# Performance work log

Measured on AMD Instinct MI355X. Metric: run time of the kernel, lower is better.

The kernel has to match this reference:

```python
import jax, jax.numpy as jnp
import numpy as np

C = 256
K = 9
PAD = (K - 1) // 2  # 4


def setup_inputs() -> dict:
    key = jax.random.key(0)
    k1, k2, k3 = jax.random.split(key, 3)
    fea = jax.random.normal(k1, (8, C, 128, 128), dtype=jnp.float32)
    # Conv2d(C, C, (1,9)) with kernel height 1 -> 1D conv weight [O, I, K]
    fan_in = C * K
    bound = 1.0 / np.sqrt(fan_in)
    weight = jax.random.uniform(k2, (C, C, K), dtype=jnp.float32, minval=-bound, maxval=bound)
    bias = jax.random.uniform(k3, (C,), dtype=jnp.float32, minval=-bound, maxval=bound)
    return {"fea": fea, "weight": weight, "bias": bias}


def _conv_relu(x, weight, bias):
    # x: [n, c, w] -> 1D conv along width, then ReLU (matches Conv2d (1,9) on a 1-row slice)
    y = jax.lax.conv_general_dilated(
        x, weight, window_strides=(1,), padding=[(PAD, PAD)],
        dimension_numbers=("NCW", "OIW", "NCW"))
    return jax.nn.relu(y + bias[None, :, None])


def reference(fea, weight, bias):
    n, c, h, w = fea.shape
    rows = jnp.moveaxis(fea, 2, 0)  # [h, n, c, w]

    def step(carry, row):
        new = _conv_relu(carry, weight, bias) + row
        return new, new

    # forward (top-down) scan: fea_stack[i] = conv(fea_stack[i-1]) + fea_stack[i]
    _, ys_f = jax.lax.scan(step, rows[0], rows[1:])
    full = jnp.concatenate([rows[:1], ys_f], axis=0)  # [h, n, c, w]

    # backward (bottom-up) scan over i = h-2 .. 1
    mid = full[1:h - 1]
    _, ys_b = jax.lax.scan(step, full[h - 1], mid[::-1])
    out_rows = jnp.concatenate([full[:1], ys_b[::-1], full[h - 1:]], axis=0)

    return jnp.moveaxis(out_rows, 0, 2)  # back to [n, c, h, w]
```

## Files before the change

kernel.cpp:

```cpp
#include <hip/hip_runtime.h>

typedef _Float16 f16;
typedef _Float16 f16x8 __attribute__((ext_vector_type(8)));
typedef _Float16 f16x4 __attribute__((ext_vector_type(4)));
typedef float    f32x4 __attribute__((ext_vector_type(4)));
typedef float    f32x16 __attribute__((ext_vector_type(16)));
typedef unsigned long long u64;

#define N_   8
#define C_   256
#define H_   128
#define W_   128
#define K_   9
#define PAD_ 4
#define WP_  136

#define WELEMS (8*9*16*64*8)
#define XT_SZ  (N_*WP_*256)
#define XBUF_F16 (N_*WP_*512)
#define NBLK   256
#define NSTEP  253
#define LDS_BYTES (40960 + 32768 + 128)

__device__ __host__ inline int xpos(int ci, int wp) {
    int g = ((ci >> 3) + 5 * wp) & 31;
    return g * 8 + (ci & 7);
}

__global__ __launch_bounds__(256) void prep_w(const float* __restrict__ w,
                                              f16* __restrict__ wh, f16* __restrict__ wl) {
    int t = blockIdx.x * 256 + threadIdx.x;
    if (t >= WELEMS) return;
    int j = t & 7;      int q = t >> 3;
    int lane = q & 63;  q >>= 6;
    int c = q & 15;     q >>= 4;
    int k = q % 9;      int ct = q / 9;
    int co = ct * 32 + (lane & 31);
    int ci = c * 16 + (lane >> 5) * 8 + j;
    float wf = w[(co * C_ + ci) * K_ + k];
    f16 hi = (f16)wf;
    f16 lo = (f16)(wf - (float)hi);
    wh[t] = hi;  wl[t] = lo;
}

__global__ __launch_bounds__(256) void prep_x0(const float* __restrict__ fea,
                                               f16* __restrict__ xb0, f16* __restrict__ xb1) {
    int t = blockIdx.x * 256 + threadIdx.x;
    if (t >= XT_SZ) return;
    int ci = t & 255;
    int wp = (t >> 8) % WP_;
    int n  = t / (WP_ * 256);
    int w  = wp - PAD_;
    bool pad = (unsigned)w >= (unsigned)W_;
    float v = pad ? 0.0f : fea[((size_t)(n * C_ + ci) * H_ + 0) * W_ + w];
    f16 hi = (f16)v;
    f16 lo = (f16)(v - (float)hi);
    size_t row = ((size_t)n * WP_ + wp) * 512;
    int p = xpos(ci, wp);
    xb0[row + p] = hi;  xb0[row + 256 + p] = lo;
    if (pad) { xb1[row + p] = (f16)0.f; xb1[row + 256 + p] = (f16)0.f; }
}

__global__ __launch_bounds__(256) void copy_row0(const float* __restrict__ fea,
                                                 float* __restrict__ out) {
    int idx = blockIdx.x * 256 + threadIdx.x;
    if (idx >= N_ * C_ * W_) return;
    int w = idx % W_;
    int nc = idx / W_;
    size_t off = (size_t)nc * (H_ * W_) + w;
    out[off] = fea[off];
}

#define TIE(x) asm volatile("" : "+v"(x))

__global__ __launch_bounds__(512, 2)
void conv_persist(
    f16* __restrict__ xb0, f16* __restrict__ xb1,
    const f16* __restrict__ whp, const f16* __restrict__ wlp,
    const float* __restrict__ bias, const float* __restrict__ fea,
    float* out, unsigned* ctr)
{
    extern __shared__ unsigned char Xs[];
    f32x4*    red  = (f32x4*)(Xs + 40960);
    unsigned* wcnt = (unsigned*)(Xs + 40960 + 32768);

    const int b   = blockIdx.x;
    const int n   = b & 7;
    const int ct  = (b >> 3) & 7;
    const int wq  = b >> 6;
    const int w0  = wq * 32;
    const int tid = threadIdx.x;
    const int wv  = tid >> 6;
    const int l   = tid & 63;
    const int m   = l & 31;
    const int hh  = l >> 5;
    unsigned* flags = ctr + n * 64;
    const int bslot = b >> 3;

    if (tid == 0) *wcnt = 0;

    f16x8 wkh[9][2], wkl[9][2];
    #pragma unroll
    for (int k = 0; k < 9; ++k)
        #pragma unroll
        for (int cs = 0; cs < 2; ++cs) {
            size_t o = ((((size_t)ct * 9 + k) * 16 + (wv * 2 + cs)) * 64 + l) * 8;
            wkh[k][cs] = *(const f16x8*)&whp[o];
            wkl[k][cs] = *(const f16x8*)&wlp[o];
        }
    #pragma unroll
    for (int k = 0; k < 9; ++k)
        #pragma unroll
        for (int cs = 0; cs < 2; ++cs) { TIE(wkh[k][cs]); TIE(wkl[k][cs]); }
    __syncthreads();

    const int dq = wv & 3;
    const int co_base = ct * 32 + dq * 8 + hh * 4;
    const size_t HW = (size_t)H_ * W_;
    float4 bv = *(const float4*)&bias[co_base];
    const float bvr[4] = {bv.x, bv.y, bv.z, bv.w};

    for (int step = 0; step < NSTEP; ++step) {
        const int  cur   = step & 1;
        const bool fwd   = step < 127;
        const int  h_out = fwd ? (step + 1) : (NSTEP - step);
        const float* radd = fwd ? fea : out;
        const size_t obase = (((size_t)(n * C_ + co_base)) * H_ + h_out) * W_ + w0 + m;
        f16* xcur = cur ? xb1 : xb0;
        f16* xnxt = cur ? xb0 : xb1;

        {
            const u64* src = (const u64*)(xcur + ((size_t)n * WP_ + w0) * 512);
            u64 va[5], vb2[5];
            #pragma unroll
            for (int ii = 0; ii < 5; ++ii) {
                int g = tid + ii * 512;
                va[ii]  = __hip_atomic_load(src + (size_t)g * 2,     __ATOMIC_RELAXED, __HIP_MEMORY_SCOPE_AGENT);
                vb2[ii] = __hip_atomic_load(src + (size_t)g * 2 + 1, __ATOMIC_RELAXED, __HIP_MEMORY_SCOPE_AGENT);
            }
            #pragma unroll
            for (int ii = 0; ii < 5; ++ii) {
                int g = tid + ii * 512;
                u64 p[2] = {va[ii], vb2[ii]};
                uint4 qd;
                __builtin_memcpy(&qd, p, 16);
                *(uint4*)(Xs + (size_t)g * 16) = qd;
            }
        }
        float rv[4] = {0.f, 0.f, 0.f, 0.f};
        if (wv < 4) {
            #pragma unroll
            for (int c2 = 0; c2 < 4; ++c2)
                rv[c2] = radd[obase + (size_t)c2 * HW];
        }
        __syncthreads();

        f32x16 a0v{}, crv{};
        #pragma unroll
        for (int k = 0; k < 9; ++k) {
            #pragma unroll
            for (int cs = 0; cs < 2; ++cs) {
                const int rl  = m + k;
                const int gsw = (((wv * 2 + cs) * 2 + hh + 5 * rl) & 31) * 16;
                const unsigned char* base = Xs + rl * 1024 + gsw;
                f16x8 bh = *(const f16x8*)base;
                f16x8 bl = *(const f16x8*)(base + 512);
                a0v = __builtin_amdgcn_mfma_f32_32x32x16_f16(wkh[k][cs], bh, a0v, 0, 0, 0);
                crv = __builtin_amdgcn_mfma_f32_32x32x16_f16(wkh[k][cs], bl, crv, 0, 0, 0);
                crv = __builtin_amdgcn_mfma_f32_32x32x16_f16(wkl[k][cs], bh, crv, 0, 0, 0);
            }
        }

        {
            f32x16 sp = a0v + crv;
            #pragma unroll
            for (int rq = 0; rq < 4; ++rq) {
                f32x4 qv = {sp[rq * 4 + 0], sp[rq * 4 + 1], sp[rq * 4 + 2], sp[rq * 4 + 3]};
                red[(wv * 4 + rq) * 64 + l] = qv;
            }
        }
        __syncthreads();

        if (wv < 4) {
            f32x4 s4 = red[(0 * 4 + dq) * 64 + l];
            #pragma unroll
            for (int cc = 1; cc < 8; ++cc)
                s4 += red[(cc * 4 + dq) * 64 + l];
            float y[4];
            #pragma unroll
            for (int c2 = 0; c2 < 4; ++c2)
                y[c2] = fmaxf(s4[c2] + bvr[c2], 0.0f) + rv[c2];

            if (step < NSTEP - 1) {
                const int wp = w0 + m + PAD_;
                const size_t row = ((size_t)n * WP_ + wp) * 512;
                const int g   = (ct * 4 + dq + 5 * wp) & 31;
                const int pos = g * 8 + hh * 4;
                f16x4 hv, lv;
                #pragma unroll
                for (int c2 = 0; c2 < 4; ++c2) {
                    f16 hi = (f16)y[c2];
                    hv[c2] = hi;
                    lv[c2] = (f16)(y[c2] - (float)hi);
                }
                u64 uh, ul;
                __builtin_memcpy(&uh, &hv, 8);
                __builtin_memcpy(&ul, &lv, 8);
                __hip_atomic_store((u64*)&xnxt[row + pos],       uh, __ATOMIC_RELAXED, __HIP_MEMORY_SCOPE_AGENT);
                __hip_atomic_store((u64*)&xnxt[row + 256 + pos], ul, __ATOMIC_RELAXED, __HIP_MEMORY_SCOPE_AGENT);
                asm volatile("s_waitcnt vmcnt(0)" ::: "memory");
                if (l == 0)
                    __hip_atomic_fetch_add(wcnt, 1u, __ATOMIC_RELAXED, __HIP_MEMORY_SCOPE_WORKGROUP);
                const unsigned tgt = (unsigned)(step + 1);
                if (wv == 0 && l == 0) {
                    while (__hip_atomic_load(wcnt, __ATOMIC_RELAXED, __HIP_MEMORY_SCOPE_WORKGROUP) < 4u * tgt) {}
                    __hip_atomic_store(flags + bslot, tgt, __ATOMIC_RELAXED, __HIP_MEMORY_SCOPE_AGENT);
                }
                #pragma unroll
                for (int c2 = 0; c2 < 4; ++c2)
                    out[obase + (size_t)c2 * HW] = y[c2];
                if (wv == 0) {
                    while (true) {
                        unsigned v = tgt;
                        if (l < 32)
                            v = __hip_atomic_load(flags + l, __ATOMIC_RELAXED, __HIP_MEMORY_SCOPE_AGENT);
                        if (__all((int)(v >= tgt))) break;
                    }
                }
            } else {
                #pragma unroll
                for (int c2 = 0; c2 < 4; ++c2)
                    out[obase + (size_t)c2 * HW] = y[c2];
            }
        }
        __syncthreads();
    }
}

__global__ __launch_bounds__(256) void step_f32(
    const float* __restrict__ xprev, const float* __restrict__ radd,
    float* __restrict__ yout, const float* __restrict__ wsrc,
    const float* __restrict__ bias, int h_prev, int h_out)
{
    __shared__ float XsF[C_][40];
    const int t  = threadIdx.x;
    const int bx = blockIdx.x;
    const int n  = bx & 7;
    const int wb = (bx >> 3) & 3;
    const int cb = bx >> 5;
    const int w0 = wb * 32;
    {
        const size_t nbase = (size_t)n * C_ * (H_ * W_) + (size_t)h_prev * W_;
        for (int idx = t; idx < C_ * 40; idx += 256) {
            int ci = idx / 40;
            int j  = idx - ci * 40;
            int w  = w0 - PAD_ + j;
            float v = 0.0f;
            if ((unsigned)w < (unsigned)W_)
                v = xprev[nbase + (size_t)ci * (H_ * W_) + w];
            XsF[ci][j] = v;
        }
    }
    __syncthreads();
    const int co = cb * 32 + (t >> 3);
    const int w4 = (t & 7) * 4;
    const float* wr = wsrc + (size_t)co * (C_ * K_);
    float acc0 = 0.f, acc1 = 0.f, acc2 = 0.f, acc3 = 0.f;
    for (int ci = 0; ci < C_; ci++) {
        float wk[K_];
        #pragma unroll
        for (int k = 0; k < K_; k++) wk[k] = wr[ci * K_ + k];
        float xv[12];
        float4 a = *(const float4*)&XsF[ci][w4];
        float4 bq = *(const float4*)&XsF[ci][w4 + 4];
        float4 c = *(const float4*)&XsF[ci][w4 + 8];
        xv[0]=a.x; xv[1]=a.y; xv[2]=a.z; xv[3]=a.w;
        xv[4]=bq.x; xv[5]=bq.y; xv[6]=bq.z; xv[7]=bq.w;
        xv[8]=c.x; xv[9]=c.y; xv[10]=c.z; xv[11]=c.w;
        #pragma unroll
        for (int k = 0; k < K_; k++) {
            acc0 = fmaf(wk[k], xv[k],     acc0);
            acc1 = fmaf(wk[k], xv[k + 1], acc1);
            acc2 = fmaf(wk[k], xv[k + 2], acc2);
            acc3 = fmaf(wk[k], xv[k + 3], acc3);
        }
    }
    const float bb = bias[co];
    const size_t obase = (((size_t)n * C_ + co) * H_ + h_out) * W_ + w0 + w4;
    float4 r = *(const float4*)&radd[obase];
    float4 o;
    o.x = fmaxf(acc0 + bb, 0.f) + r.x;
    o.y = fmaxf(acc1 + bb, 0.f) + r.y;
    o.z = fmaxf(acc2 + bb, 0.f) + r.z;
    o.w = fmaxf(acc3 + bb, 0.f) + r.w;
    *(float4*)&yout[obase] = o;
}

extern "C" void kernel_launch(void* const* d_in, const int* in_sizes, int n_in,
                              void* d_out, int out_size, void* d_ws, size_t ws_size,
                              hipStream_t stream) {
    const float* fea    = (const float*)d_in[0];
    const float* weight = (const float*)d_in[1];
    const float* bias   = (const float*)d_in[2];
    float* out = (float*)d_out;

    const size_t need = (size_t)2 * WELEMS * 2 + (size_t)2 * XBUF_F16 * 2 + 2048;

    copy_row0<<<(N_ * C_ * W_ + 255) / 256, 256, 0, stream>>>(fea, out);

    if (ws_size >= need && d_ws != nullptr) {
        f16* wh  = (f16*)d_ws;
        f16* wl  = wh + WELEMS;
        f16* xb0 = wl + WELEMS;
        f16* xb1 = xb0 + XBUF_F16;
        unsigned* ctr = (unsigned*)(xb1 + XBUF_F16);

        hipMemsetAsync(ctr, 0, 2048, stream);
        prep_w<<<(WELEMS + 255) / 256, 256, 0, stream>>>(weight, wh, wl);
        prep_x0<<<(XT_SZ + 255) / 256, 256, 0, stream>>>(fea, xb0, xb1);

        hipFuncSetAttribute((const void*)conv_persist,
                            hipFuncAttributeMaxDynamicSharedMemorySize, LDS_BYTES);
        conv_persist<<<NBLK, 512, LDS_BYTES, stream>>>(xb0, xb1, wh, wl, bias, fea, out, ctr);
    } else {
        for (int h = 1; h < H_; h++)
            step_f32<<<256, 256, 0, stream>>>(out, fea, out, weight, bias, h - 1, h);
        for (int h = H_ - 2; h >= 1; h--)
            step_f32<<<256, 256, 0, stream>>>(out, out, out, weight, bias, h + 1, h);
    }
}
```

Baseline: 1.341 ms.

## Split hi/lo activation staging into two LDS phases to overlap compute

Per step, the hi half of the activation window is written to LDS first and the hi-dependent MFMAs (wh*xh, wl*xh) run, then the lo half is stored to a separate LDS region and the wh*xl MFMAs run. This lets the lo stores sit behind the first MFMA batch and splits the single compensation accumulator into two independent chains. It adds a barrier per step, keeps more registers live across the first MFMA phase, and enlarges the LDS footprint, which could hurt occupancy with two blocks per CU.

After: 1.494 ms. +11.4%, slower.

```diff
diff --git a/kernel.cpp b/kernel.cpp
--- a/kernel.cpp
+++ b/kernel.cpp
@@ -20,7 +20,10 @@
 #define XBUF_F16 (N_*WP_*512)
 #define NBLK   256
 #define NSTEP  253
-#define LDS_BYTES (40960 + 32768 + 128)
+#define XS_LO  20480
+#define RED_OFF 40960
+#define WCNT_OFF 73728
+#define LDS_BYTES 84992
 
 __device__ __host__ inline int xpos(int ci, int wp) {
     int g = ((ci >> 3) + 5 * wp) & 31;
@@ -81,8 +84,8 @@
     float* out, unsigned* ctr)
 {
     extern __shared__ unsigned char Xs[];
-    f32x4*    red  = (f32x4*)(Xs + 40960);
-    unsigned* wcnt = (unsigned*)(Xs + 40960 + 32768);
+    f32x4*    red  = (f32x4*)(Xs + RED_OFF);
+    unsigned* wcnt = (unsigned*)(Xs + WCNT_OFF);
 
     const int b   = blockIdx.x;
     const int n   = b & 7;
@@ -129,23 +132,14 @@
         f16* xcur = cur ? xb1 : xb0;
         f16* xnxt = cur ? xb0 : xb1;
 
-        {
-            const u64* src = (const u64*)(xcur + ((size_t)n * WP_ + w0) * 512);
-            u64 va[5], vb2[5];
-            #pragma unroll
-            for (int ii = 0; ii < 5; ++ii) {
-                int g = tid + ii * 512;
-                va[ii]  = __hip_atomic_load(src + (size_t)g * 2,     __ATOMIC_RELAXED, __HIP_MEMORY_SCOPE_AGENT);
-                vb2[ii] = __hip_atomic_load(src + (size_t)g * 2 + 1, __ATOMIC_RELAXED, __HIP_MEMORY_SCOPE_AGENT);
-            }
-            #pragma unroll
-            for (int ii = 0; ii < 5; ++ii) {
-                int g = tid + ii * 512;
-                u64 p[2] = {va[ii], vb2[ii]};
-                uint4 qd;
-                __builtin_memcpy(&qd, p, 16);
-                *(uint4*)(Xs + (size_t)g * 16) = qd;
-            }
+        const u64* src = (const u64*)(xcur + ((size_t)n * WP_ + w0) * 512);
+        u64 vhi[5], vlo[5];
+        #pragma unroll
+        for (int ii = 0; ii < 5; ++ii) {
+            int idx = tid + ii * 512;
+            int row = idx >> 6, g = idx & 63;
+            vhi[ii] = __hip_atomic_load(src + (size_t)row * 128 + g,      __ATOMIC_RELAXED, __HIP_MEMORY_SCOPE_AGENT);
+            vlo[ii] = __hip_atomic_load(src + (size_t)row * 128 + 64 + g, __ATOMIC_RELAXED, __HIP_MEMORY_SCOPE_AGENT);
         }
         float rv[4] = {0.f, 0.f, 0.f, 0.f};
         if (wv < 4) {
@@ -153,26 +147,47 @@
             for (int c2 = 0; c2 < 4; ++c2)
                 rv[c2] = radd[obase + (size_t)c2 * HW];
         }
+        #pragma unroll
+        for (int ii = 0; ii < 5; ++ii) {
+            int idx = tid + ii * 512;
+            int row = idx >> 6, g = idx & 63;
+            *(u64*)(Xs + row * 512 + g * 8) = vhi[ii];
+        }
         __syncthreads();
 
-        f32x16 a0v{}, crv{};
+        f32x16 a0v{}, c1v{}, c2v{};
         #pragma unroll
         for (int k = 0; k < 9; ++k) {
             #pragma unroll
             for (int cs = 0; cs < 2; ++cs) {
                 const int rl  = m + k;
                 const int gsw = (((wv * 2 + cs) * 2 + hh + 5 * rl) & 31) * 16;
-                const unsigned char* base = Xs + rl * 1024 + gsw;
-                f16x8 bh = *(const f16x8*)base;
-                f16x8 bl = *(const f16x8*)(base + 512);
+                f16x8 bh = *(const f16x8*)(Xs + rl * 512 + gsw);
                 a0v = __builtin_amdgcn_mfma_f32_32x32x16_f16(wkh[k][cs], bh, a0v, 0, 0, 0);
-                crv = __builtin_amdgcn_mfma_f32_32x32x16_f16(wkh[k][cs], bl, crv, 0, 0, 0);
-                crv = __builtin_amdgcn_mfma_f32_32x32x16_f16(wkl[k][cs], bh, crv, 0, 0, 0);
+                c2v = __builtin_amdgcn_mfma_f32_32x32x16_f16(wkl[k][cs], bh, c2v, 0, 0, 0);
             }
         }
+        #pragma unroll
+        for (int ii = 0; ii < 5; ++ii) {
+            int idx = tid + ii * 512;
+            int row = idx >> 6, g = idx & 63;
+            *(u64*)(Xs + XS_LO + row * 512 + g * 8) = vlo[ii];
+        }
+        __syncthreads();
+
+        #pragma unroll
+        for (int k = 0; k < 9; ++k) {
+            #pragma unroll
+            for (int cs = 0; cs < 2; ++cs) {
+                const int rl  = m + k;
+                const int gsw = (((wv * 2 + cs) * 2 + hh + 5 * rl) & 31) * 16;
+                f16x8 bl = *(const f16x8*)(Xs + XS_LO + rl * 512 + gsw);
+                c1v = __builtin_amdgcn_mfma_f32_32x32x16_f16(wkh[k][cs], bl, c1v, 0, 0, 0);
+            }
+        }
 
         {
-            f32x16 sp = a0v + crv;
+            f32x16 sp = (a0v + c1v) + c2v;
             #pragma unroll
             for (int rq = 0; rq < 4; ++rq) {
                 f32x4 qv = {sp[rq * 4 + 0], sp[rq * 4 + 1], sp[rq * 4 + 2], sp[rq * 4 + 3]};
```

## Double block to 1024 threads, split channel reduction and roles across waves

Applied to the files above, without the earlier changes.

Each block now runs 16 waves, and each wave handles a single 16-input-channel chunk with one accumulator. This shortens the per-wave MFMA chain and the per-step critical path. Partial sums are reduced in two stages through LDS. Output stores, next-buffer stores with flag signalling, and the cross-block flag polling are assigned to separate wave groups so they overlap. It adds an extra barrier per step and more register pressure per CU.

Result: slower. 1.700 ms (+26.8%).

```diff
diff --git a/kernel.cpp b/kernel.cpp
--- a/kernel.cpp
+++ b/kernel.cpp
@@ -20,7 +20,9 @@
 #define XBUF_F16 (N_*WP_*512)
 #define NBLK   256
 #define NSTEP  253
-#define LDS_BYTES (40960 + 32768 + 128)
+#define RED_OFF  40960
+#define WCNT_OFF 73728
+#define LDS_BYTES 84992
 
 __device__ __host__ inline int xpos(int ci, int wp) {
     int g = ((ci >> 3) + 5 * wp) & 31;
@@ -73,7 +75,7 @@
 
 #define TIE(x) asm volatile("" : "+v"(x))
 
-__global__ __launch_bounds__(512, 2)
+__global__ __launch_bounds__(1024, 4)
 void conv_persist(
     f16* __restrict__ xb0, f16* __restrict__ xb1,
     const f16* __restrict__ whp, const f16* __restrict__ wlp,
@@ -81,8 +83,8 @@
     float* out, unsigned* ctr)
 {
     extern __shared__ unsigned char Xs[];
-    f32x4*    red  = (f32x4*)(Xs + 40960);
-    unsigned* wcnt = (unsigned*)(Xs + 40960 + 32768);
+    f32x4*    red  = (f32x4*)(Xs + RED_OFF);
+    unsigned* wcnt = (unsigned*)(Xs + WCNT_OFF);
 
     const int b   = blockIdx.x;
     const int n   = b & 7;
@@ -99,19 +101,15 @@
 
     if (tid == 0) *wcnt = 0;
 
-    f16x8 wkh[9][2], wkl[9][2];
+    f16x8 wkh[9], wkl[9];
     #pragma unroll
-    for (int k = 0; k < 9; ++k)
-        #pragma unroll
-        for (int cs = 0; cs < 2; ++cs) {
-            size_t o = ((((size_t)ct * 9 + k) * 16 + (wv * 2 + cs)) * 64 + l) * 8;
-            wkh[k][cs] = *(const f16x8*)&whp[o];
-            wkl[k][cs] = *(const f16x8*)&wlp[o];
-        }
+    for (int k = 0; k < 9; ++k) {
+        size_t o = ((((size_t)ct * 9 + k) * 16 + wv) * 64 + l) * 8;
+        wkh[k] = *(const f16x8*)&whp[o];
+        wkl[k] = *(const f16x8*)&wlp[o];
+    }
     #pragma unroll
-    for (int k = 0; k < 9; ++k)
-        #pragma unroll
-        for (int cs = 0; cs < 2; ++cs) { TIE(wkh[k][cs]); TIE(wkl[k][cs]); }
+    for (int k = 0; k < 9; ++k) { TIE(wkh[k]); TIE(wkl[k]); }
     __syncthreads();
 
     const int dq = wv & 3;
@@ -131,57 +129,56 @@
 
         {
             const u64* src = (const u64*)(xcur + ((size_t)n * WP_ + w0) * 512);
-            u64 va[5], vb2[5];
-            #pragma unroll
-            for (int ii = 0; ii < 5; ++ii) {
-                int g = tid + ii * 512;
-                va[ii]  = __hip_atomic_load(src + (size_t)g * 2,     __ATOMIC_RELAXED, __HIP_MEMORY_SCOPE_AGENT);
-                vb2[ii] = __hip_atomic_load(src + (size_t)g * 2 + 1, __ATOMIC_RELAXED, __HIP_MEMORY_SCOPE_AGENT);
-            }
-            #pragma unroll
-            for (int ii = 0; ii < 5; ++ii) {
-                int g = tid + ii * 512;
-                u64 p[2] = {va[ii], vb2[ii]};
-                uint4 qd;
-                __builtin_memcpy(&qd, p, 16);
-                *(uint4*)(Xs + (size_t)g * 16) = qd;
-            }
+            u64 v[5];
+            #pragma unroll
+            for (int ii = 0; ii < 5; ++ii)
+                v[ii] = __hip_atomic_load(src + (size_t)(tid + ii * 1024),
+                                          __ATOMIC_RELAXED, __HIP_MEMORY_SCOPE_AGENT);
+            #pragma unroll
+            for (int ii = 0; ii < 5; ++ii)
+                *(u64*)(Xs + (size_t)(tid + ii * 1024) * 8) = v[ii];
         }
         float rv[4] = {0.f, 0.f, 0.f, 0.f};
-        if (wv < 4) {
+        if (wv < 8) {
             #pragma unroll
             for (int c2 = 0; c2 < 4; ++c2)
                 rv[c2] = radd[obase + (size_t)c2 * HW];
         }
         __syncthreads();
 
-        f32x16 a0v{}, crv{};
+        f32x16 a{};
         #pragma unroll
         for (int k = 0; k < 9; ++k) {
-            #pragma unroll
-            for (int cs = 0; cs < 2; ++cs) {
-                const int rl  = m + k;
-                const int gsw = (((wv * 2 + cs) * 2 + hh + 5 * rl) & 31) * 16;
-                const unsigned char* base = Xs + rl * 1024 + gsw;
-                f16x8 bh = *(const f16x8*)base;
-                f16x8 bl = *(const f16x8*)(base + 512);
-                a0v = __builtin_amdgcn_mfma_f32_32x32x16_f16(wkh[k][cs], bh, a0v, 0, 0, 0);
-                crv = __builtin_amdgcn_mfma_f32_32x32x16_f16(wkh[k][cs], bl, crv, 0, 0, 0);
-                crv = __builtin_amdgcn_mfma_f32_32x32x16_f16(wkl[k][cs], bh, crv, 0, 0, 0);
+            const int rl  = m + k;
+            const int gsw = ((wv * 2 + hh + 5 * rl) & 31) * 16;
+            const unsigned char* base = Xs + rl * 1024 + gsw;
+            f16x8 bh = *(const f16x8*)base;
+            f16x8 bl = *(const f16x8*)(base + 512);
+            a = __builtin_amdgcn_mfma_f32_32x32x16_f16(wkh[k], bh, a, 0, 0, 0);
+            a = __builtin_amdgcn_mfma_f32_32x32x16_f16(wkh[k], bl, a, 0, 0, 0);
+            a = __builtin_amdgcn_mfma_f32_32x32x16_f16(wkl[k], bh, a, 0, 0, 0);
+        }
+
+        if (wv >= 8) {
+            #pragma unroll
+            for (int rq = 0; rq < 4; ++rq) {
+                f32x4 qv = {a[rq * 4 + 0], a[rq * 4 + 1], a[rq * 4 + 2], a[rq * 4 + 3]};
+                red[((wv - 8) * 4 + rq) * 64 + l] = qv;
             }
         }
-
-        {
-            f32x16 sp = a0v + crv;
+        __syncthreads();
+
+        if (wv < 8) {
             #pragma unroll
             for (int rq = 0; rq < 4; ++rq) {
-                f32x4 qv = {sp[rq * 4 + 0], sp[rq * 4 + 1], sp[rq * 4 + 2], sp[rq * 4 + 3]};
-                red[(wv * 4 + rq) * 64 + l] = qv;
+                f32x4 qv = {a[rq * 4 + 0], a[rq * 4 + 1], a[rq * 4 + 2], a[rq * 4 + 3]};
+                red[(wv * 4 + rq) * 64 + l] = qv + red[(wv * 4 + rq) * 64 + l];
             }
         }
         __syncthreads();
 
-        if (wv < 4) {
+        const unsigned tgt = (unsigned)(step + 1);
+        if (wv < 8) {
             f32x4 s4 = red[(0 * 4 + dq) * 64 + l];
             #pragma unroll
             for (int cc = 1; cc < 8; ++cc)
@@ -191,7 +188,11 @@
             for (int c2 = 0; c2 < 4; ++c2)
                 y[c2] = fmaxf(s4[c2] + bvr[c2], 0.0f) + rv[c2];
 
-            if (step < NSTEP - 1) {
+            if (wv < 4) {
+                #pragma unroll
+                for (int c2 = 0; c2 < 4; ++c2)
+                    out[obase + (size_t)c2 * HW] = y[c2];
+            } else if (step < NSTEP - 1) {
                 const int wp = w0 + m + PAD_;
                 const size_t row = ((size_t)n * WP_ + wp) * 512;
                 const int g   = (ct * 4 + dq + 5 * wp) & 31;
@@ -211,26 +212,17 @@
                 asm volatile("s_waitcnt vmcnt(0)" ::: "memory");
                 if (l == 0)
                     __hip_atomic_fetch_add(wcnt, 1u, __ATOMIC_RELAXED, __HIP_MEMORY_SCOPE_WORKGROUP);
-                const unsigned tgt = (unsigned)(step + 1);
-                if (wv == 0 && l == 0) {
+                if (wv == 4 && l == 0) {
                     while (__hip_atomic_load(wcnt, __ATOMIC_RELAXED, __HIP_MEMORY_SCOPE_WORKGROUP) < 4u * tgt) {}
                     __hip_atomic_store(flags + bslot, tgt, __ATOMIC_RELAXED, __HIP_MEMORY_SCOPE_AGENT);
                 }
-                #pragma unroll
-                for (int c2 = 0; c2 < 4; ++c2)
-                    out[obase + (size_t)c2 * HW] = y[c2];
-                if (wv == 0) {
-                    while (true) {
-                        unsigned v = tgt;
-                        if (l < 32)
-                            v = __hip_atomic_load(flags + l, __ATOMIC_RELAXED, __HIP_MEMORY_SCOPE_AGENT);
-                        if (__all((int)(v >= tgt))) break;
-                    }
-                }
-            } else {
-                #pragma unroll
-                for (int c2 = 0; c2 < 4; ++c2)
-                    out[obase + (size_t)c2 * HW] = y[c2];
+            }
+        } else if (wv == 8 && step < NSTEP - 1) {
+            while (true) {
+                unsigned v = tgt;
+                if (l < 32)
+                    v = __hip_atomic_load(flags + l, __ATOMIC_RELAXED, __HIP_MEMORY_SCOPE_AGENT);
+                if (__all((int)(v >= tgt))) break;
             }
         }
         __syncthreads();
@@ -321,7 +313,7 @@
 
         hipFuncSetAttribute((const void*)conv_persist,
                             hipFuncAttributeMaxDynamicSharedMemorySize, LDS_BYTES);
-        conv_persist<<<NBLK, 512, LDS_BYTES, stream>>>(xb0, xb1, wh, wl, bias, fea, out, ctr);
+        conv_persist<<<NBLK, 1024, LDS_BYTES, stream>>>(xb0, xb1, wh, wl, bias, fea, out, ctr);
     } else {
         for (int h = 1; h < H_; h++)
             step_f32<<<256, 256, 0, stream>>>(out, fea, out, weight, bias, h - 1, h);
```
